# Kernel optimization log

Measured on AMD Instinct MI355X. Metric: run time of the kernel, lower is better.

Reference implementation:

```python
import jax, jax.numpy as jnp
import numpy as np

NUM_HEADS = 16
D_MODEL = 1024
HEAD_DIM = D_MODEL // NUM_HEADS  # 64
NEG_INF = -1e9


def alibi_bidirectional_bias(num_heads, seq_len, dtype=jnp.float32):
    """[num_heads, S, S] bias: first H/2 heads forward-causal ALiBi, last H/2 backward."""
    half = num_heads // 2
    base = 24.0 ** (1.0 / half)
    slopes = (1.0 / base ** jnp.arange(1, half + 1, dtype=dtype))[:, None, None]  # [half,1,1]
    pos = jnp.arange(seq_len)
    rel = (pos[None, :] - pos[:, None]).astype(dtype)  # rel[i,j] = j - i
    neg = jnp.full((seq_len, seq_len), NEG_INF, dtype=dtype)
    fwd = slopes * jnp.tril(rel) + jnp.triu(neg, 1)          # causal (attend past)
    bwd = slopes * jnp.triu(-rel) + jnp.tril(neg, -1)        # anti-causal (attend future)
    return jnp.concatenate([fwd, bwd], axis=0)  # [H, S, S]


def setup_inputs() -> dict:
    key = jax.random.key(0)
    ks = jax.random.split(key, 9)
    B, S, D = 2, 2048, D_MODEL
    sc = 1.0 / np.sqrt(D)
    inp = {"x": jax.random.normal(ks[0], (B, S, D), dtype=jnp.float32)}
    inp["Wq"] = jax.random.normal(ks[1], (D, D), dtype=jnp.float32) * sc
    inp["bq"] = jnp.zeros((D,), dtype=jnp.float32)
    inp["Wk"] = jax.random.normal(ks[2], (D, D), dtype=jnp.float32) * sc
    inp["bk"] = jnp.zeros((D,), dtype=jnp.float32)
    inp["Wv"] = jax.random.normal(ks[3], (D, D), dtype=jnp.float32) * sc
    inp["bv"] = jnp.zeros((D,), dtype=jnp.float32)
    inp["Wf"] = jax.random.normal(ks[4], (D, D), dtype=jnp.float32) * sc
    inp["bf"] = jnp.zeros((D,), dtype=jnp.float32)
    return inp


def reference(x, Wq, bq, Wk, bk, Wv, bv, Wf, bf):
    B, S, D = x.shape
    H, hd = NUM_HEADS, HEAD_DIM

    def heads(y):  # [B,S,D] -> [B,H,S,hd]
        return y.reshape(B, S, H, hd).transpose(0, 2, 1, 3)

    q = heads(x @ Wq + bq)
    k = heads(x @ Wk + bk)
    v = heads(x @ Wv + bv)

    bias = alibi_bidirectional_bias(H, S, x.dtype)  # [H,S,S]
    scores = jnp.einsum("bhqd,bhkd->bhqk", q, k) * (1.0 / np.sqrt(hd)) + bias[None]
    attn = jax.nn.softmax(scores, axis=-1)
    out = jnp.einsum("bhqk,bhkd->bhqd", attn, v)
    out = out.transpose(0, 2, 1, 3).reshape(B, S, D)
    return out @ Wf + bf
```

## Files before the change

### kernel.cpp

```cpp
#include <hip/hip_runtime.h>

#define S_LEN 2048
#define NH 16
#define HD 64
#define DM 1024
#define BSZ 2

typedef __bf16 bf16;
typedef __bf16 bf16x8 __attribute__((ext_vector_type(8)));
typedef float f32x4 __attribute__((ext_vector_type(4)));
typedef const unsigned int __attribute__((address_space(1)))* gas_ptr;
typedef unsigned int __attribute__((address_space(3)))* las_ptr;

__device__ __forceinline__ void gl_lds16(const bf16* g, bf16* l) {
  __builtin_amdgcn_global_load_lds((gas_ptr)g, (las_ptr)l, 16, 0, 0);
}

#define CFENCE asm volatile("" ::: "memory")

__global__ __launch_bounds__(256) void k_prep(
    const float* __restrict__ x, bf16* __restrict__ xb,
    const float* __restrict__ W0, const float* __restrict__ W1,
    const float* __restrict__ W2, const float* __restrict__ W3,
    bf16* __restrict__ dqkv, bf16* __restrict__ df) {
  __shared__ float t[64][65];
  const int id = blockIdx.x;
  if (id < 4096) {
    int i = id * 256 + threadIdx.x;
    float4 v = ((const float4*)x)[i];
    union { ushort4 u; bf16 b[4]; } o;
    o.b[0] = (bf16)v.x; o.b[1] = (bf16)v.y; o.b[2] = (bf16)v.z; o.b[3] = (bf16)v.w;
    ((ushort4*)xb)[i] = o.u;
    return;
  }
  const int id2 = id - 4096;
  const int z = id2 >> 8;
  const float* W = (z == 0) ? W0 : (z == 1) ? W1 : (z == 2) ? W2 : W3;
  bf16* D = (z < 3) ? (dqkv + (size_t)z * 1048576) : df;
  int k0 = ((id2 >> 4) & 15) * 64, n0 = (id2 & 15) * 64;
  int c = threadIdx.x & 63, rr = threadIdx.x >> 6;
#pragma unroll
  for (int it = 0; it < 16; ++it) {
    int r = it * 4 + rr;
    t[r][c] = W[(size_t)(k0 + r) * DM + n0 + c];
  }
  __syncthreads();
#pragma unroll
  for (int it = 0; it < 16; ++it) {
    int r = it * 4 + rr;
    D[(size_t)(n0 + r) * DM + k0 + c] = (bf16)t[c][r];
  }
}

template <int MODE, int BM, int BN>
__global__ __launch_bounds__(256) void k_gemm(
    const bf16* __restrict__ A, const bf16* __restrict__ Bt,
    const float* __restrict__ b0, const float* __restrict__ b1,
    const float* __restrict__ b2, void* __restrict__ Cout,
    bf16* __restrict__ VtOut, int M, int N, int K) {
  __shared__ __align__(16) bf16 As[BM * 64];
  __shared__ __align__(16) bf16 Bs[BN * 64];
  constexpr int MIc = BM / 32, NIc = BN / 32;
  const int tid = threadIdx.x;
  const int l = tid & 63, w = tid >> 6;
  const int lm = l & 15, lg = l >> 4;
  const int bm = blockIdx.x * BM, bn = blockIdx.y * BN;
  const int wm = (w >> 1) * (BM / 2), wn = (w & 1) * (BN / 2);

  f32x4 acc[MIc][NIc] = {};
  const bf16* Ag = A + (size_t)bm * K;
  const bf16* Bg = Bt + (size_t)bn * K;

  for (int k0 = 0; k0 < K; k0 += 64) {
#pragma unroll
    for (int it = 0; it < BM / 32; ++it) {
      int cl = it * 256 + tid;
      int row = cl >> 3;
      int cs = ((cl & 7) ^ (row & 7)) << 3;
      gl_lds16(Ag + (size_t)row * K + k0 + cs, &As[(it * 256 + w * 64) * 8]);
    }
#pragma unroll
    for (int it = 0; it < BN / 32; ++it) {
      int cl = it * 256 + tid;
      int row = cl >> 3;
      int cs = ((cl & 7) ^ (row & 7)) << 3;
      gl_lds16(Bg + (size_t)row * K + k0 + cs, &Bs[(it * 256 + w * 64) * 8]);
    }
    __syncthreads();
#pragma unroll
    for (int kk = 0; kk < 2; ++kk) {
      bf16x8 af[MIc], bfr[NIc];
#pragma unroll
      for (int mi = 0; mi < MIc; ++mi) {
        int row = wm + mi * 16 + lm;
        af[mi] = *(const bf16x8*)&As[row * 64 + ((((kk << 2) + lg) ^ (row & 7)) << 3)];
      }
#pragma unroll
      for (int ni = 0; ni < NIc; ++ni) {
        int row = wn + ni * 16 + lm;
        bfr[ni] = *(const bf16x8*)&Bs[row * 64 + ((((kk << 2) + lg) ^ (row & 7)) << 3)];
      }
#pragma unroll
      for (int mi = 0; mi < MIc; ++mi)
#pragma unroll
        for (int ni = 0; ni < NIc; ++ni)
          acc[mi][ni] = __builtin_amdgcn_mfma_f32_16x16x32_bf16(
              af[mi], bfr[ni], acc[mi][ni], 0, 0, 0);
    }
    __syncthreads();
  }

#pragma unroll
  for (int ni = 0; ni < NIc; ++ni) {
    int n = bn + wn + ni * 16 + lm;
    float bv;
    if (MODE == 0) {
      const float* bp = (n < 1024) ? b0 : (n < 2048) ? b1 : b2;
      bv = bp[n & 1023];
    } else {
      bv = b0[n];
    }
#pragma unroll
    for (int mi = 0; mi < MIc; ++mi) {
#pragma unroll
      for (int r = 0; r < 4; ++r) {
        int m = bm + wm + mi * 16 + lg * 4 + r;
        float v = acc[mi][ni][r] + bv;
        if (MODE == 0) {
          int qkv = n >> 10;
          int h = (n >> 6) & 15;
          int d = n & 63;
          int b = m >> 11, s = m & 2047;
          if (qkv == 2) {
            VtOut[((size_t)(b * NH + h) * HD + d) * S_LEN + s] = (bf16)v;
          } else {
            ((bf16*)Cout)[(size_t)qkv * (BSZ * NH * S_LEN * HD) +
                          ((size_t)(b * NH + h) * S_LEN + s) * HD + d] = (bf16)v;
          }
        } else {
          ((float*)Cout)[(size_t)m * N + n] = v;
        }
      }
    }
  }
}

#define SMX(MASKED)                                                           \
  {                                                                           \
    const float t0 = slp2 * (float)dlo;                                       \
    _Pragma("unroll") for (int ni = 0; ni < 4; ++ni) {                        \
      const int koff = (ni & 1) * 32 + (ni >> 1) * 4;                         \
      float bni = t0 + dni[ni];                                               \
      float pr[4];                                                            \
      _Pragma("unroll") for (int r = 0; r < 4; ++r) {                         \
        float v = fmaf(sc[ni][r], c1, bni + srr[r]);                          \
        if (MASKED) {                                                         \
          int reli = dlo + koff + relc + r;                                   \
          bool ok = causal ? (reli <= 0) : (reli >= 0);                       \
          v = ok ? v : -1e9f;                                                 \
        }                                                                     \
        pr[r] = __builtin_amdgcn_exp2f(v);                                    \
      }                                                                       \
      union { bf16 b[2]; unsigned u; } u0, u1;                                \
      u0.b[0] = (bf16)pr[0]; u0.b[1] = (bf16)pr[1];                           \
      u1.b[0] = (bf16)pr[2]; u1.b[1] = (bf16)pr[3];                           \
      pk[ni][0] = u0.u; pk[ni][1] = u1.u;                                     \
    }                                                                         \
  }

__global__ __launch_bounds__(512, 2) void k_attn(const bf16* __restrict__ Qh,
                                                 const bf16* __restrict__ Kh,
                                                 const bf16* __restrict__ Vt,
                                                 bf16* __restrict__ O) {
  __shared__ __align__(16) bf16 Ks[2][4096];
  __shared__ __align__(16) bf16 Vs[2][4096];
  const int id = blockIdx.x;
  const int bh = ((id & 7) << 2) | ((id >> 3) & 3);
  const int pid = id >> 5;
  const int b = bh >> 4, h = bh & 15;
  const bool causal = (h < 8);
  const int tid = threadIdx.x;
  const int w = tid >> 6, l = tid & 63;
  const int lm = l & 15, lg = l >> 4;
  const int hh = causal ? h : h - 8;
  const float c1 = 0.18033688f;
  const float sm = __builtin_amdgcn_exp2f(-(float)(hh + 1) * 0.57312035f) * 1.44269504f;
  const float slp2 = causal ? sm : -sm;
  const int relc = lg * 8 - lm;
  const int krow_lane = ((lm >> 2) << 3) + (lm & 3);
  const int swzK = (lm & 3) | (((lm >> 2) & 1) << 2);
  const int swzV = (lm & 3) | (((lm >> 3) & 1) << 2);
  float dni[4], srr[4];
#pragma unroll
  for (int ni = 0; ni < 4; ++ni)
    dni[ni] = slp2 * (float)((ni & 1) * 32 + (ni >> 1) * 4);
#pragma unroll
  for (int r = 0; r < 4; ++r) srr[r] = slp2 * (float)(relc + r);

  const bf16* Qp = Qh + (size_t)bh * S_LEN * HD;
  const bf16* Kp = Kh + (size_t)bh * S_LEN * HD;
  const bf16* Vp = Vt + (size_t)bh * HD * S_LEN;

  bf16x8 ones;
#pragma unroll
  for (int i = 0; i < 8; ++i) ones[i] = (bf16)1.0f;

  auto stage = [&](bf16* lk, bf16* lv, int j0) {
    const int row = tid >> 3, c = tid & 7;
    const int sw = (row & 3) | (((row >> 3) & 1) << 2);
    const int gc = (c ^ sw) << 3;
    const int clb8 = ((tid >> 6) << 6) * 8;
    gl_lds16(Kp + (size_t)(j0 + row) * HD + gc, lk + clb8);
    gl_lds16(Vp + (size_t)row * S_LEN + j0 + gc, lv + clb8);
  };

  auto run_strip = [&](int yi) {
    const int qb = yi << 7;
    const int q0 = qb + w * 16;
    const int jbase = causal ? 0 : qb;
    const int jcnt = causal ? (qb >> 6) + 2 : ((S_LEN - qb) >> 6);

    bf16x8 qf[2];
#pragma unroll
    for (int kk = 0; kk < 2; ++kk)
      qf[kk] = *(const bf16x8*)&Qp[(size_t)(q0 + lm) * HD + kk * 32 + lg * 8];

    f32x4 oacc[4] = {};
    f32x4 lacc = {};

    auto compute = [&](int t, const bf16* lk, const bf16* lv) {
      const int j0 = jbase + t * 64;
      const int dlo = j0 - q0;
      const bool skip = causal ? (dlo >= 16) : (dlo <= -64);
      if (skip) return;
      f32x4 sc[4] = {};
#pragma unroll
      for (int kk = 0; kk < 2; ++kk)
#pragma unroll
        for (int ni = 0; ni < 4; ++ni) {
          const int koff = (ni & 1) * 32 + (ni >> 1) * 4;
          bf16x8 kf = *(const bf16x8*)&lk[(koff + krow_lane) * 64 +
                                          ((((kk << 2) + lg) ^ swzK) << 3)];
          sc[ni] = __builtin_amdgcn_mfma_f32_16x16x32_bf16(kf, qf[kk], sc[ni],
                                                           0, 0, 0);
        }
      bf16x8 vf[2][4];
#pragma unroll
      for (int kk = 0; kk < 2; ++kk)
#pragma unroll
        for (int di = 0; di < 4; ++di)
          vf[kk][di] = *(const bf16x8*)&lv[(di * 16 + lm) * 64 +
                                           ((((kk << 2) + lg) ^ swzV) << 3)];
      const bool full = causal ? (dlo <= -63) : (dlo >= 15);
      unsigned pk[4][2];
      if (full) { SMX(false); } else { SMX(true); }
#pragma unroll
      for (int kk = 0; kk < 2; ++kk) {
        union { unsigned d[4]; bf16x8 v; } pa;
        pa.d[0] = pk[kk][0];
        pa.d[1] = pk[kk][1];
        pa.d[2] = pk[kk + 2][0];
        pa.d[3] = pk[kk + 2][1];
        lacc = __builtin_amdgcn_mfma_f32_16x16x32_bf16(pa.v, ones, lacc, 0, 0, 0);
#pragma unroll
        for (int di = 0; di < 4; ++di)
          oacc[di] = __builtin_amdgcn_mfma_f32_16x16x32_bf16(pa.v, vf[kk][di],
                                                             oacc[di], 0, 0, 0);
      }
    };

    stage(Ks[0], Vs[0], jbase);
    asm volatile("s_waitcnt vmcnt(0)" ::: "memory");
    __builtin_amdgcn_s_barrier();
    CFENCE;

    for (int t = 0; t < jcnt - 1; ++t) {
      const int cur = t & 1;
      stage(Ks[cur ^ 1], Vs[cur ^ 1], jbase + (t + 1) * 64);
      asm volatile("s_waitcnt vmcnt(2)" ::: "memory");
      __builtin_amdgcn_s_barrier();
      CFENCE;
      compute(t, Ks[cur], Vs[cur]);
      CFENCE;
      __builtin_amdgcn_s_barrier();
      CFENCE;
    }
    asm volatile("s_waitcnt vmcnt(0)" ::: "memory");
    __builtin_amdgcn_s_barrier();
    CFENCE;
    compute(jcnt - 1, Ks[(jcnt - 1) & 1], Vs[(jcnt - 1) & 1]);
    CFENCE;
    __builtin_amdgcn_s_barrier();
    CFENCE;

    float rin[4];
#pragma unroll
    for (int r = 0; r < 4; ++r) rin[r] = 1.0f / lacc[r];
#pragma unroll
    for (int di = 0; di < 4; ++di) {
      int d = h * HD + di * 16 + lm;
#pragma unroll
      for (int r = 0; r < 4; ++r) {
        int q = q0 + lg * 4 + r;
        O[((size_t)b * S_LEN + q) * DM + d] = (bf16)(oacc[di][r] * rin[r]);
      }
    }
  };

  run_strip(pid);
  run_strip(15 - pid);
}

extern "C" void kernel_launch(void* const* d_in, const int* in_sizes, int n_in,
                              void* d_out, int out_size, void* d_ws, size_t ws_size,
                              hipStream_t stream) {
  const float* x  = (const float*)d_in[0];
  const float* Wq = (const float*)d_in[1];
  const float* bq = (const float*)d_in[2];
  const float* Wk = (const float*)d_in[3];
  const float* bk = (const float*)d_in[4];
  const float* Wv = (const float*)d_in[5];
  const float* bv = (const float*)d_in[6];
  const float* Wf = (const float*)d_in[7];
  const float* bfp = (const float*)d_in[8];

  char* ws = (char*)d_ws;
  const size_t MB = 1ull << 20;
  bf16* xb    = (bf16*)(ws);
  bf16* Wqkvt = (bf16*)(ws + 8 * MB);
  bf16* Wft   = (bf16*)(ws + 14 * MB);
  bf16* QKVh  = (bf16*)(ws + 16 * MB);
  bf16* Vt    = (bf16*)(ws + 40 * MB);
  bf16* O     = QKVh + 2 * 4194304;

  k_prep<<<5120, 256, 0, stream>>>(x, xb, Wq, Wk, Wv, Wf, Wqkvt, Wft);
  k_gemm<0, 128, 128><<<dim3(32, 24), 256, 0, stream>>>(
      xb, Wqkvt, bq, bk, bv, QKVh, Vt, 4096, 3072, 1024);
  k_attn<<<256, 512, 0, stream>>>(QKVh, QKVh + 4194304, Vt, O);
  k_gemm<2, 64, 128><<<dim3(64, 8), 256, 0, stream>>>(
      O, Wft, bfp, bfp, bfp, d_out, nullptr, 4096, 1024, 1024);
}
```

Baseline: 186.1 us.

## Double-buffer GEMM LDS tiles, remap blocks per XCD, stage V transpose via LDS

The GEMM kernel now double-buffers its A/B LDS tiles so the next K-tile's global-to-LDS loads are in flight while the current tile is multiplied, using explicit vmcnt waits and barriers. Block indices are remapped from a 1D grid so that blocks landing on the same XCD share A/B tiles for better L2 reuse. The V-transpose epilogue is also reworked: values are staged through a swizzled LDS buffer and then written as coalesced 16-byte stores instead of strided scalar stores. This doubles LDS use per block, which may lower occupancy, and the hardcoded vmcnt values and grid mapping assume these exact shapes.

```diff
diff --git a/kernel.cpp b/kernel.cpp
--- a/kernel.cpp
+++ b/kernel.cpp
@@ -58,35 +58,65 @@
     const float* __restrict__ b0, const float* __restrict__ b1,
     const float* __restrict__ b2, void* __restrict__ Cout,
     bf16* __restrict__ VtOut, int M, int N, int K) {
-  __shared__ __align__(16) bf16 As[BM * 64];
-  __shared__ __align__(16) bf16 Bs[BN * 64];
+  constexpr int NST = BM / 32 + BN / 32;
+  __shared__ __align__(16) bf16 SA[2][BM * 64];
+  __shared__ __align__(16) bf16 SB[2][BN * 64];
   constexpr int MIc = BM / 32, NIc = BN / 32;
   const int tid = threadIdx.x;
   const int l = tid & 63, w = tid >> 6;
   const int lm = l & 15, lg = l >> 4;
-  const int bm = blockIdx.x * BM, bn = blockIdx.y * BN;
+  const int id = blockIdx.x;
+  const int xcd = id & 7, r2 = id >> 3;
+  int bx, by;
+  if (MODE == 0) {
+    bx = (xcd & 3) * 8 + (r2 & 7);
+    by = (xcd >> 2) * 12 + (r2 >> 3);
+  } else {
+    bx = (xcd & 3) * 16 + (r2 & 15);
+    by = (xcd >> 2) * 4 + (r2 >> 4);
+  }
+  const int bm = bx * BM, bn = by * BN;
   const int wm = (w >> 1) * (BM / 2), wn = (w & 1) * (BN / 2);
 
   f32x4 acc[MIc][NIc] = {};
   const bf16* Ag = A + (size_t)bm * K;
   const bf16* Bg = Bt + (size_t)bn * K;
 
-  for (int k0 = 0; k0 < K; k0 += 64) {
+  auto stage = [&](int k0, int bufi) {
 #pragma unroll
     for (int it = 0; it < BM / 32; ++it) {
       int cl = it * 256 + tid;
       int row = cl >> 3;
       int cs = ((cl & 7) ^ (row & 7)) << 3;
-      gl_lds16(Ag + (size_t)row * K + k0 + cs, &As[(it * 256 + w * 64) * 8]);
+      gl_lds16(Ag + (size_t)row * K + k0 + cs, &SA[bufi][(it * 256 + w * 64) * 8]);
     }
 #pragma unroll
     for (int it = 0; it < BN / 32; ++it) {
       int cl = it * 256 + tid;
       int row = cl >> 3;
       int cs = ((cl & 7) ^ (row & 7)) << 3;
-      gl_lds16(Bg + (size_t)row * K + k0 + cs, &Bs[(it * 256 + w * 64) * 8]);
-    }
-    __syncthreads();
+      gl_lds16(Bg + (size_t)row * K + k0 + cs, &SB[bufi][(it * 256 + w * 64) * 8]);
+    }
+  };
+
+  stage(0, 0);
+  const int nk = K >> 6;
+  int buf = 0;
+  for (int t = 0; t < nk; ++t) {
+    if (t + 1 < nk) {
+      stage((t + 1) << 6, buf ^ 1);
+      if constexpr (NST == 8) {
+        asm volatile("s_waitcnt vmcnt(8)" ::: "memory");
+      } else {
+        asm volatile("s_waitcnt vmcnt(6)" ::: "memory");
+      }
+    } else {
+      asm volatile("s_waitcnt vmcnt(0)" ::: "memory");
+    }
+    __builtin_amdgcn_s_barrier();
+    CFENCE;
+    const bf16* As = SA[buf];
+    const bf16* Bs = SB[buf];
 #pragma unroll
     for (int kk = 0; kk < 2; ++kk) {
       bf16x8 af[MIc], bfr[NIc];
@@ -107,7 +137,41 @@
           acc[mi][ni] = __builtin_amdgcn_mfma_f32_16x16x32_bf16(
               af[mi], bfr[ni], acc[mi][ni], 0, 0, 0);
     }
+    CFENCE;
+    __builtin_amdgcn_s_barrier();
+    CFENCE;
+    buf ^= 1;
+  }
+
+  if (MODE == 0 && bn >= 2048) {
+    bf16* sc = (bf16*)SA;
+#pragma unroll
+    for (int ni = 0; ni < NIc; ++ni) {
+      int n_l = wn + ni * 16 + lm;
+      float bv = b2[(bn + n_l) & 1023];
+#pragma unroll
+      for (int mi = 0; mi < MIc; ++mi) {
+        int g = ((wm + mi * 16) >> 2) + lg;
+        int gp = g ^ ((n_l & 7) << 2);
+        union { ushort4 u; bf16 bb[4]; } pkv;
+#pragma unroll
+        for (int r = 0; r < 4; ++r) pkv.bb[r] = (bf16)(acc[mi][ni][r] + bv);
+        *(ushort4*)&sc[n_l * 128 + gp * 4] = pkv.u;
+      }
+    }
     __syncthreads();
+    const int bq = bm >> 11, s0 = bm & 2047;
+#pragma unroll
+    for (int it2 = 0; it2 < 8; ++it2) {
+      int row = it2 * 16 + (tid >> 4), c = tid & 15;
+      int g0p = (2 * c) ^ ((row & 7) << 2);
+      float4 val = *(const float4*)&sc[row * 128 + g0p * 4];
+      int ng = bn + row;
+      int hV = (ng >> 6) & 15;
+      int d = ng & 63;
+      *(float4*)&VtOut[((size_t)(bq * NH + hV) * HD + d) * S_LEN + s0 + c * 8] = val;
+    }
+    return;
   }
 
 #pragma unroll
@@ -115,8 +179,7 @@
     int n = bn + wn + ni * 16 + lm;
     float bv;
     if (MODE == 0) {
-      const float* bp = (n < 1024) ? b0 : (n < 2048) ? b1 : b2;
-      bv = bp[n & 1023];
+      bv = (n < 1024) ? b0[n] : b1[n & 1023];
     } else {
       bv = b0[n];
     }
@@ -131,12 +194,8 @@
           int h = (n >> 6) & 15;
           int d = n & 63;
           int b = m >> 11, s = m & 2047;
-          if (qkv == 2) {
-            VtOut[((size_t)(b * NH + h) * HD + d) * S_LEN + s] = (bf16)v;
-          } else {
-            ((bf16*)Cout)[(size_t)qkv * (BSZ * NH * S_LEN * HD) +
-                          ((size_t)(b * NH + h) * S_LEN + s) * HD + d] = (bf16)v;
-          }
+          ((bf16*)Cout)[(size_t)qkv * (BSZ * NH * S_LEN * HD) +
+                        ((size_t)(b * NH + h) * S_LEN + s) * HD + d] = (bf16)v;
         } else {
           ((float*)Cout)[(size_t)m * N + n] = v;
         }
@@ -334,9 +393,9 @@
   bf16* O     = QKVh + 2 * 4194304;
 
   k_prep<<<5120, 256, 0, stream>>>(x, xb, Wq, Wk, Wv, Wf, Wqkvt, Wft);
-  k_gemm<0, 128, 128><<<dim3(32, 24), 256, 0, stream>>>(
+  k_gemm<0, 128, 128><<<768, 256, 0, stream>>>(
       xb, Wqkvt, bq, bk, bv, QKVh, Vt, 4096, 3072, 1024);
   k_attn<<<256, 512, 0, stream>>>(QKVh, QKVh + 4194304, Vt, O);
-  k_gemm<2, 64, 128><<<dim3(64, 8), 256, 0, stream>>>(
+  k_gemm<2, 64, 128><<<512, 256, 0, stream>>>(
       O, Wft, bfp, bfp, bfp, d_out, nullptr, 4096, 1024, 1024);
 }
```

Result: no change. 182.8 us (-1.8%).
